# Kernel tuning notes

Hardware: AMD Instinct MI355X
Metric: run time of the kernel (lower is better)

Reference implementation:

```python
import jax, jax.numpy as jnp
import numpy as np

B, T, D, H = 8192, 64, 100, 110  # batch, t_grid_size, W_dim, 10+W_dim
S = T - 1                        # number of subnets / loop steps
SIG, R, DCOEF = 0.3, 0.1, 0.1
NUM_TIME_INTERVAL = 1.0
EPS = 1e-6


def setup_inputs() -> dict:
    key = jax.random.key(0)
    ks = jax.random.split(key, 16)
    f32 = jnp.float32
    inp = {
        "W": jax.random.normal(ks[0], (B, T, D), f32),
        "y_init": jax.random.uniform(ks[1], (1,), f32, 0.0, 1.0),
        "z_init": jax.random.uniform(ks[2], (1,), f32, -0.1, 0.1),
        # BatchNorm params: gamma ~ U(0.1,0.5), beta ~ N(0, 0.1) as in the keras initializers
        "g0": jax.random.uniform(ks[3], (S, D + 1), f32, 0.1, 0.5),
        "b0": 0.1 * jax.random.normal(ks[4], (S, D + 1), f32),
        "g1": jax.random.uniform(ks[5], (S, H), f32, 0.1, 0.5),
        "b1": 0.1 * jax.random.normal(ks[6], (S, H), f32),
        "g2": jax.random.uniform(ks[7], (S, H), f32, 0.1, 0.5),
        "b2": 0.1 * jax.random.normal(ks[8], (S, H), f32),
        "g3": jax.random.uniform(ks[9], (S, D), f32, 0.1, 0.5),
        "b3": 0.1 * jax.random.normal(ks[10], (S, D), f32),
        # Dense weights (glorot-ish scale); first two have no bias, last has bias
        "w0": jax.random.normal(ks[11], (S, D + 1, H), f32) / np.sqrt(D + 1),
        "w1": jax.random.normal(ks[12], (S, H, H), f32) / np.sqrt(H),
        "w2": jax.random.normal(ks[13], (S, H, D), f32) / np.sqrt(H),
        "bias2": jnp.zeros((S, D), f32),
    }
    return inp


def _bn(z, gamma, beta):
    # training-mode batch norm over batch axis (keras axis=1 -> per-feature)
    mu = jnp.mean(z, axis=0, keepdims=True)
    var = jnp.var(z, axis=0, keepdims=True)
    return gamma * (z - mu) * jax.lax.rsqrt(var + EPS) + beta


def reference(W, y_init, z_init, g0, b0, g1, b1, g2, b2, g3, b3, w0, w1, w2, bias2):
    delta_t = NUM_TIME_INTERVAL / T
    dW = jnp.transpose(W[:, 1:, :] - W[:, :-1, :], (1, 0, 2))  # [S, B, D]
    t_idx = jnp.arange(S, dtype=W.dtype)
    exp_coef = jnp.exp(-3.0 * R * (1.0 - t_idx * delta_t))      # [S]

    x0 = jnp.full((B, D), np.pi / 2, W.dtype)
    y0 = jnp.ones((B, 1), W.dtype) * y_init
    z0 = jnp.ones((B, D), W.dtype) * z_init

    def drift(x, y, ec):
        s = jnp.sum(jnp.sin(x), axis=1, keepdims=True)
        return -R * y + 0.5 * SIG ** 2 * ec * (DCOEF * s) ** 3

    def step(carry, xs):
        x, y, z = carry
        dw, ec, pg0, pb0, pg1, pb1, pg2, pb2, pg3, pb3, pw0, pw1, pw2, pbb = xs
        x = x + SIG * dw * y
        y = y - drift(x, y, ec) * delta_t + jnp.sum(z * dw, axis=1, keepdims=True)
        h = jnp.concatenate([x, y], axis=1)          # [B, D+1]
        h = _bn(h, pg0, pb0)
        h = jax.nn.relu(_bn(h @ pw0, pg1, pb1))      # [B, H]
        h = jax.nn.relu(_bn(h @ pw1, pg2, pb2))      # [B, H]
        z = _bn(h @ pw2 + pbb, pg3, pb3) / D         # [B, D]
        return (x, y, z), None

    xs = (dW, exp_coef, g0, b0, g1, b1, g2, b2, g3, b3, w0, w1, w2, bias2)
    (x, y, z), _ = jax.lax.scan(step, (x0, y0, z0), xs)

    # final step: Python loop leaves t = T-2; increment W[:,-1]-W[:,-2] == dW[-1]
    dw_last = dW[-1]
    x = x + SIG * y * dw_last
    y = y - drift(x, y, exp_coef[-1]) * delta_t + jnp.sum(z * dw_last, axis=1, keepdims=True)
    return (x, y)
```

## Files before the change

kernel.cpp:

```cpp
#include <hip/hip_runtime.h>
#include <cstdint>
#include <cstddef>

#define NBLK 128
#define NT   256
#define ROWS 64
#define DD   100
#define HH   110
#define NS   63
#define NGRP 16
#define GRP  (NBLK / NGRP)
#define REGF 512

typedef __bf16 bf16x8 __attribute__((ext_vector_type(8)));
typedef float  f32x16 __attribute__((ext_vector_type(16)));

struct Params {
  const float* W; const float* yini; const float* zini;
  const float* g0; const float* b0; const float* g1; const float* b1;
  const float* g2; const float* b2; const float* g3; const float* b3;
  const float* w0; const float* w1; const float* w2;
  float* out; float* slots; int* cnts;
};

__device__ __forceinline__ float agent_ld(const float* p_) {
  return __hip_atomic_load(p_, __ATOMIC_RELAXED, __HIP_MEMORY_SCOPE_AGENT);
}
__device__ __forceinline__ void agent_st(float* p_, float v) {
  __hip_atomic_store(p_, v, __ATOMIC_RELAXED, __HIP_MEMORY_SCOPE_AGENT);
}

__device__ __forceinline__ void sync_arrive(int* cn) {
  asm volatile("s_waitcnt vmcnt(0)" ::: "memory");
  __syncthreads();
  if (threadIdx.x == 0)
    __hip_atomic_fetch_add(&cn[(blockIdx.x & (NGRP - 1)) * 16], 1,
                           __ATOMIC_RELAXED, __HIP_MEMORY_SCOPE_AGENT);
}
__device__ __forceinline__ void sync_wait(int* cn, int target) {
  if (threadIdx.x < NGRP) {
    while (__hip_atomic_load(&cn[threadIdx.x * 16], __ATOMIC_RELAXED,
                             __HIP_MEMORY_SCOPE_AGENT) < target)
      __builtin_amdgcn_s_sleep(1);
  }
  __syncthreads();
  asm volatile("" ::: "memory");
}

template<int K, int N>
__device__ __forceinline__ void issueB(const float* wg, int n, int half, float (*t)[8]) {
#pragma unroll
  for (int c = 0; c < 7; ++c) {
#pragma unroll
    for (int j = 0; j < 8; ++j) {
      int k = c * 16 + half * 8 + j;
      t[c][j] = (k < K && n < N) ? wg[k * N + n] : 0.f;
    }
  }
}

__device__ __forceinline__ void run_mfma2(const __bf16* hs, const float (*t)[8],
                                          int col, int half, f32x16* acc) {
  acc[0] = (f32x16)(0.f);
  acc[1] = (f32x16)(0.f);
#pragma unroll
  for (int c = 0; c < 7; ++c) {
    bf16x8 bfv;
#pragma unroll
    for (int j = 0; j < 8; ++j) bfv[j] = (__bf16)t[c][j];
    bf16x8 a0 = *(const bf16x8*)(hs + col * 120 + c * 16 + half * 8);
    bf16x8 a1 = *(const bf16x8*)(hs + (32 + col) * 120 + c * 16 + half * 8);
    acc[0] = __builtin_amdgcn_mfma_f32_32x32x16_bf16(a0, bfv, acc[0], 0, 0, 0);
    acc[1] = __builtin_amdgcn_mfma_f32_32x32x16_bf16(a1, bfv, acc[1], 0, 0, 0);
  }
}

__device__ __forceinline__ void frag2(const f32x16* acc, float* slot, int n, int N, int half) {
  float sm = 0.f, sq = 0.f;
#pragma unroll
  for (int m = 0; m < 2; ++m)
#pragma unroll
    for (int i = 0; i < 16; ++i) { float v = acc[m][i]; sm += v; sq += v * v; }
  sm += __shfl_xor(sm, 32);
  sq += __shfl_xor(sq, 32);
  if (half == 0 && n < N) {
    atomicAdd(&slot[n], sm);
    atomicAdd(&slot[112 + n], sq);
  }
}

__device__ __forceinline__ void frag3(const f32x16* acc, float* slot, int n, int half,
                                      const float* ysl) {
  float sm = 0.f, sq = 0.f, sy = 0.f;
#pragma unroll
  for (int m = 0; m < 2; ++m)
#pragma unroll
    for (int i = 0; i < 16; ++i) {
      float v = acc[m][i];
      int row = m * 32 + (i & 3) + 8 * (i >> 2) + 4 * half;
      sm += v; sq += v * v; sy += v * ysl[row];
    }
  sm += __shfl_xor(sm, 32);
  sq += __shfl_xor(sq, 32);
  sy += __shfl_xor(sy, 32);
  if (half == 0 && n < HH) {
    atomicAdd(&slot[n], sm);
    atomicAdd(&slot[112 + n], sq);
    atomicAdd(&slot[224 + n], sy);
  }
}

__device__ __forceinline__ void finalize2(const float* slot, const float* gam,
                                          const float* bet, int n, int N, float scale,
                                          float& a, float& c) {
  a = 0.f; c = 0.f;
  if (n < N) {
    float sm = agent_ld(&slot[n]);
    float sq = agent_ld(&slot[112 + n]);
    float mean = sm * (1.f / 8192.f);
    float var  = fmaxf(sq * (1.f / 8192.f) - mean * mean, 0.f);
    float au = gam[n] * rsqrtf(var + 1e-6f);
    a = au * scale;
    c = (bet[n] - mean * au) * scale;
  }
}

__device__ __forceinline__ void write_h(__bf16* hs, const f32x16* acc,
                                        float a, float c, int n, int half) {
  if (n < 112) {
#pragma unroll
    for (int m = 0; m < 2; ++m)
#pragma unroll
      for (int i = 0; i < 16; ++i) {
        int row = m * 32 + (i & 3) + 8 * (i >> 2) + 4 * half;
        float v = fmaxf(acc[m][i] * a + c, 0.f);
        hs[row * 120 + n] = (__bf16)v;
      }
  }
}

__device__ __forceinline__ void write_h1(__bf16* hs, const f32x16* acc,
                                         float a, float c, float ay, float cy,
                                         float w0yn, int n, int half, const float* ysl) {
  if (n < 112) {
#pragma unroll
    for (int m = 0; m < 2; ++m)
#pragma unroll
      for (int i = 0; i < 16; ++i) {
        int row = m * 32 + (i & 3) + 8 * (i >> 2) + 4 * half;
        float add = (ay * ysl[row] + cy) * w0yn;
        float v = fmaxf((acc[m][i] + add) * a + c, 0.f);
        hs[row * 120 + n] = (__bf16)v;
      }
  }
}

__device__ __forceinline__ void write_z(float* zsl, const f32x16* acc,
                                        float a, float c, int n, int half) {
  if (n < DD) {
#pragma unroll
    for (int m = 0; m < 2; ++m)
#pragma unroll
      for (int i = 0; i < 16; ++i) {
        int row = m * 32 + (i & 3) + 8 * (i >> 2) + 4 * half;
        zsl[row * 104 + n] = acc[m][i] * a + c;
      }
  }
}

__global__ __launch_bounds__(NT) void bsde_kernel(Params p) {
  __shared__ float xs[ROWS * 104];
  __shared__ float zs[ROWS * 104];
  __shared__ float dws[ROWS * 104];
  __shared__ float ys[ROWS];
  __shared__ float us[ROWS];
  __shared__ __bf16 hsb[ROWS * 120];
  __shared__ float aS[128], cS[128];

  const int tid  = threadIdx.x;
  const int lane = tid & 63;
  const int wv   = tid >> 6;
  const int col  = lane & 31;
  const int half = lane >> 5;
  const int n    = wv * 32 + col;
  const int b0   = blockIdx.x * ROWS;

  {
    float z0 = p.zini[0];
    for (int i = tid; i < ROWS * 104; i += NT) { xs[i] = 1.57079632679f; zs[i] = z0; }
    for (int i = tid; i < ROWS * 120; i += NT) hsb[i] = (__bf16)0.f;
    if (tid < ROWS) ys[tid] = p.yini[0];
  }
  for (int idx = tid; idx < ROWS * 128; idx += NT) {
    int r = idx >> 7, d = idx & 127;
    if (d < DD) {
      const float* wr = p.W + (size_t)(b0 + r) * 6400 + d;
      dws[r * 104 + d] = wr[100] - wr[0];
    }
  }
  __syncthreads();

  int seg = 0;
  float tB[7][8];
  float w0yn;

  {
    int r = tid >> 2, l4 = tid & 3;
    float yr = ys[r];
    float ssum = 0.f;
#pragma unroll
    for (int i = 0; i < 25; ++i) {
      int d = l4 + 4 * i;
      float dw = dws[r * 104 + d];
      float xv = xs[r * 104 + d] + 0.3f * dw * yr;
      xs[r * 104 + d] = xv;
      ssum += __sinf(xv);
    }
    ssum += __shfl_down(ssum, 2, 4);
    ssum += __shfl_down(ssum, 1, 4);
    if (l4 == 0) {
      float ec = __expf(-0.3f);
      float tc = 0.1f * ssum;
      float drift = -0.1f * yr + 0.045f * ec * tc * tc * tc;
      us[r] = yr - drift * (1.f / 64.f);
    }
  }
  __syncthreads();
  {
    float* slot = p.slots + (seg % 3) * REGF;
    if (tid < DD) {
      float sm = 0.f, sq = 0.f;
      for (int r = 0; r < ROWS; ++r) { float v = xs[r * 104 + tid]; sm += v; sq += v * v; }
      atomicAdd(&slot[224 + tid], sm);
      atomicAdd(&slot[336 + tid], sq);
    }
    sync_arrive(p.cnts);
    issueB<DD, HH>(p.w0, n, half, tB);
    w0yn = (n < HH) ? p.w0[100 * 110 + n] : 0.f;
    sync_wait(p.cnts, (seg + 1) * GRP);
    if (blockIdx.x < 2)
      agent_st(&p.slots[((seg + 2) % 3) * REGF + (int)blockIdx.x * 256 + tid], 0.f);
    if (tid < DD) {
      float sm = agent_ld(&slot[224 + tid]);
      float sq = agent_ld(&slot[336 + tid]);
      float mean = sm * (1.f / 8192.f);
      float var  = fmaxf(sq * (1.f / 8192.f) - mean * mean, 0.f);
      float au = p.g0[tid] * rsqrtf(var + 1e-6f);
      aS[tid] = au; cS[tid] = p.b0[tid] - mean * au;
    }
    ++seg;
  }
  __syncthreads();

  for (int s = 0; s < NS; ++s) {
    {
      int r = tid >> 2, l4 = tid & 3;
      float zdw = 0.f;
#pragma unroll
      for (int i = 0; i < 25; ++i) {
        int d = l4 + 4 * i;
        zdw += zs[r * 104 + d] * dws[r * 104 + d];
      }
      zdw += __shfl_down(zdw, 2, 4);
      zdw += __shfl_down(zdw, 1, 4);
      if (l4 == 0) ys[r] = us[r] + zdw;
    }
    __syncthreads();
    float* Eslot = p.slots + (seg % 3) * REGF;
    if (tid < 64) {
      float v = ys[tid], v2 = v * v;
#pragma unroll
      for (int off = 32; off > 0; off >>= 1) {
        v  += __shfl_down(v, off);
        v2 += __shfl_down(v2, off);
      }
      if (tid == 0) { atomicAdd(&Eslot[336], v); atomicAdd(&Eslot[337], v2); }
    }
    for (int idx = tid; idx < ROWS * 128; idx += NT) {
      int r = idx >> 7, d = idx & 127;
      if (d < DD) hsb[r * 120 + d] = (__bf16)(xs[r * 104 + d] * aS[d] + cS[d]);
    }
    __syncthreads();

    f32x16 acc[2];
    run_mfma2(hsb, tB, col, half, acc);
    frag3(acc, Eslot, n, half, ys);
    sync_arrive(p.cnts);
    issueB<HH, HH>(p.w1 + (size_t)s * 12100, n, half, tB);
    sync_wait(p.cnts, (seg + 1) * GRP);
    if (blockIdx.x < 2)
      agent_st(&p.slots[((seg + 2) % 3) * REGF + (int)blockIdx.x * 256 + tid], 0.f);
    float ay, cy, a1 = 0.f, c1 = 0.f;
    {
      float Sy  = agent_ld(&Eslot[336]);
      float Syy = agent_ld(&Eslot[337]);
      float my = Sy * (1.f / 8192.f);
      float vy = fmaxf(Syy * (1.f / 8192.f) - my * my, 0.f);
      float auy = p.g0[s * 101 + 100] * rsqrtf(vy + 1e-6f);
      ay = auy; cy = p.b0[s * 101 + 100] - my * auy;
      if (n < HH) {
        float G1 = agent_ld(&Eslot[n]);
        float G2 = agent_ld(&Eslot[112 + n]);
        float G3 = agent_ld(&Eslot[224 + n]);
        float Sv  = ay * Sy + 8192.f * cy;
        float Svv = ay * ay * Syy + 2.f * ay * cy * Sy + 8192.f * cy * cy;
        float w = w0yn;
        float S1 = G1 + w * Sv;
        float S2 = G2 + 2.f * w * (ay * G3 + cy * G1) + w * w * Svv;
        float mean = S1 * (1.f / 8192.f);
        float var  = fmaxf(S2 * (1.f / 8192.f) - mean * mean, 0.f);
        float au = p.g1[s * HH + n] * rsqrtf(var + 1e-6f);
        a1 = au; c1 = p.b1[s * HH + n] - mean * au;
      }
    }
    ++seg;
    write_h1(hsb, acc, a1, c1, ay, cy, w0yn, n, half, ys);
    __syncthreads();

    run_mfma2(hsb, tB, col, half, acc);
    float* Cslot = p.slots + (seg % 3) * REGF;
    frag2(acc, Cslot, n, HH, half);
    sync_arrive(p.cnts);
    issueB<HH, DD>(p.w2 + (size_t)s * 11000, n, half, tB);
    if (s + 1 < NS) {
      for (int idx = tid; idx < ROWS * 128; idx += NT) {
        int r = idx >> 7, d = idx & 127;
        if (d < DD) {
          const float* wr = p.W + (size_t)(b0 + r) * 6400 + (s + 1) * 100 + d;
          dws[r * 104 + d] = wr[100] - wr[0];
        }
      }
      w0yn = (n < HH) ? p.w0[(size_t)(s + 1) * 11110 + 11000 + n] : 0.f;
    }
    sync_wait(p.cnts, (seg + 1) * GRP);
    if (blockIdx.x < 2)
      agent_st(&p.slots[((seg + 2) % 3) * REGF + (int)blockIdx.x * 256 + tid], 0.f);
    float a2, c2;
    finalize2(Cslot, p.g2 + s * HH, p.b2 + s * HH, n, HH, 1.f, a2, c2);
    ++seg;
    write_h(hsb, acc, a2, c2, n, half);
    __syncthreads();
    run_mfma2(hsb, tB, col, half, acc);
    float* Dslot = p.slots + (seg % 3) * REGF;
    frag2(acc, Dslot, n, DD, half);
    {
      int r = tid >> 2, l4 = tid & 3;
      float yr = ys[r];
      float ssum = 0.f;
#pragma unroll
      for (int i = 0; i < 25; ++i) {
        int d = l4 + 4 * i;
        float dw = dws[r * 104 + d];
        float xv = xs[r * 104 + d] + 0.3f * dw * yr;
        xs[r * 104 + d] = xv;
        ssum += __sinf(xv);
      }
      ssum += __shfl_down(ssum, 2, 4);
      ssum += __shfl_down(ssum, 1, 4);
      if (l4 == 0) {
        int ei = (s + 1 < NS) ? s + 1 : NS - 1;
        float ec = __expf(-0.3f * (1.f - (float)ei * (1.f / 64.f)));
        float tc = 0.1f * ssum;
        float drift = -0.1f * yr + 0.045f * ec * tc * tc * tc;
        us[r] = yr - drift * (1.f / 64.f);
      }
    }
    __syncthreads();
    if (tid < DD) {
      float sm = 0.f, sq = 0.f;
      for (int r = 0; r < ROWS; ++r) { float v = xs[r * 104 + tid]; sm += v; sq += v * v; }
      atomicAdd(&Dslot[224 + tid], sm);
      atomicAdd(&Dslot[336 + tid], sq);
    }
    sync_arrive(p.cnts);
    if (s + 1 < NS) issueB<DD, HH>(p.w0 + (size_t)(s + 1) * 11110, n, half, tB);
    sync_wait(p.cnts, (seg + 1) * GRP);
    if (blockIdx.x < 2)
      agent_st(&p.slots[((seg + 2) % 3) * REGF + (int)blockIdx.x * 256 + tid], 0.f);
    float a3, c3;
    finalize2(Dslot, p.g3 + s * DD, p.b3 + s * DD, n, DD, 0.01f, a3, c3);
    if (s + 1 < NS && tid < DD) {
      float sm = agent_ld(&Dslot[224 + tid]);
      float sq = agent_ld(&Dslot[336 + tid]);
      float mean = sm * (1.f / 8192.f);
      float var  = fmaxf(sq * (1.f / 8192.f) - mean * mean, 0.f);
      float au = p.g0[(s + 1) * 101 + tid] * rsqrtf(var + 1e-6f);
      aS[tid] = au; cS[tid] = p.b0[(s + 1) * 101 + tid] - mean * au;
    }
    ++seg;
    write_z(zs, acc, a3, c3, n, half);
    __syncthreads();
  }

  {
    int r = tid >> 2, l4 = tid & 3;
    float zdw = 0.f;
#pragma unroll
    for (int i = 0; i < 25; ++i) {
      int d = l4 + 4 * i;
      zdw += zs[r * 104 + d] * dws[r * 104 + d];
    }
    zdw += __shfl_down(zdw, 2, 4);
    zdw += __shfl_down(zdw, 1, 4);
    if (l4 == 0) ys[r] = us[r] + zdw;
  }
  __syncthreads();

  for (int idx = tid; idx < ROWS * 128; idx += NT) {
    int r = idx >> 7, d = idx & 127;
    if (d < DD) p.out[(size_t)(b0 + r) * 100 + d] = xs[r * 104 + d];
  }
  if (tid < ROWS) p.out[819200 + b0 + tid] = ys[tid];
}

extern "C" void kernel_launch(void* const* d_in, const int* in_sizes, int n_in,
                              void* d_out, int out_size, void* d_ws, size_t ws_size,
                              hipStream_t stream) {
  Params p;
  p.W    = (const float*)d_in[0];
  p.yini = (const float*)d_in[1];
  p.zini = (const float*)d_in[2];
  p.g0   = (const float*)d_in[3];  p.b0 = (const float*)d_in[4];
  p.g1   = (const float*)d_in[5];  p.b1 = (const float*)d_in[6];
  p.g2   = (const float*)d_in[7];  p.b2 = (const float*)d_in[8];
  p.g3   = (const float*)d_in[9];  p.b3 = (const float*)d_in[10];
  p.w0   = (const float*)d_in[11]; p.w1 = (const float*)d_in[12];
  p.w2   = (const float*)d_in[13];
  p.out   = (float*)d_out;
  p.slots = (float*)d_ws;
  p.cnts  = (int*)((char*)d_ws + (size_t)3 * REGF * 4);

  size_t zbytes = (size_t)3 * REGF * 4
                + (size_t)NGRP * 16 * 4;
  hipMemsetAsync(d_ws, 0, zbytes, stream);
  bsde_kernel<<<dim3(NBLK), dim3(NT), 0, stream>>>(p);
}
```

Measured before the change: 3.116 ms.

## Replace flat grid barrier with hierarchical group/super counter and release flags

Changes the grid-wide barrier from each block polling all 16 group counters with 16 threads to a two-level tree. The last arriver in each group bumps a super counter, and the final group writes per-group release flags that each block polls with a single thread. It also loads the y-statistics once per block into shared memory instead of every thread doing agent-scope loads. The aim is less polling traffic and contention on the barrier counters, at the cost of a longer serial chain of atomics on the critical arrival path.

```diff
diff --git a/kernel.cpp b/kernel.cpp
--- a/kernel.cpp
+++ b/kernel.cpp
@@ -20,7 +20,7 @@
   const float* g0; const float* b0; const float* g1; const float* b1;
   const float* g2; const float* b2; const float* g3; const float* b3;
   const float* w0; const float* w1; const float* w2;
-  float* out; float* slots; int* cnts;
+  float* out; float* slots; int* gcnt; int* scnt; int* rel;
 };
 
 __device__ __forceinline__ float agent_ld(const float* p_) {
@@ -30,17 +30,29 @@
   __hip_atomic_store(p_, v, __ATOMIC_RELAXED, __HIP_MEMORY_SCOPE_AGENT);
 }
 
-__device__ __forceinline__ void sync_arrive(int* cn) {
+__device__ __forceinline__ void sync_arrive(int* gcnt, int* scnt, int* rel, int bar) {
   asm volatile("s_waitcnt vmcnt(0)" ::: "memory");
   __syncthreads();
-  if (threadIdx.x == 0)
-    __hip_atomic_fetch_add(&cn[(blockIdx.x & (NGRP - 1)) * 16], 1,
-                           __ATOMIC_RELAXED, __HIP_MEMORY_SCOPE_AGENT);
-}
-__device__ __forceinline__ void sync_wait(int* cn, int target) {
-  if (threadIdx.x < NGRP) {
-    while (__hip_atomic_load(&cn[threadIdx.x * 16], __ATOMIC_RELAXED,
-                             __HIP_MEMORY_SCOPE_AGENT) < target)
+  if (threadIdx.x == 0) {
+    int g = blockIdx.x & (NGRP - 1);
+    int old = __hip_atomic_fetch_add(&gcnt[g * 16], 1,
+                                     __ATOMIC_RELAXED, __HIP_MEMORY_SCOPE_AGENT);
+    if (old == GRP * (bar + 1) - 1) {
+      int so = __hip_atomic_fetch_add(scnt, 1,
+                                      __ATOMIC_RELAXED, __HIP_MEMORY_SCOPE_AGENT);
+      if (so == NGRP * (bar + 1) - 1) {
+#pragma unroll
+        for (int i = 0; i < NGRP; ++i)
+          __hip_atomic_store(&rel[i * 16], bar + 1,
+                             __ATOMIC_RELAXED, __HIP_MEMORY_SCOPE_AGENT);
+      }
+    }
+  }
+}
+__device__ __forceinline__ void sync_wait(const int* rel, int bar) {
+  if (threadIdx.x == 0) {
+    while (__hip_atomic_load(&rel[(blockIdx.x & (NGRP - 1)) * 16],
+                             __ATOMIC_RELAXED, __HIP_MEMORY_SCOPE_AGENT) < bar + 1)
       __builtin_amdgcn_s_sleep(1);
   }
   __syncthreads();
@@ -176,6 +188,7 @@
   __shared__ float us[ROWS];
   __shared__ __bf16 hsb[ROWS * 120];
   __shared__ float aS[128], cS[128];
+  __shared__ float syS[2];
 
   const int tid  = threadIdx.x;
   const int lane = tid & 63;
@@ -234,10 +247,10 @@
       atomicAdd(&slot[224 + tid], sm);
       atomicAdd(&slot[336 + tid], sq);
     }
-    sync_arrive(p.cnts);
+    sync_arrive(p.gcnt, p.scnt, p.rel, seg);
     issueB<DD, HH>(p.w0, n, half, tB);
     w0yn = (n < HH) ? p.w0[100 * 110 + n] : 0.f;
-    sync_wait(p.cnts, (seg + 1) * GRP);
+    sync_wait(p.rel, seg);
     if (blockIdx.x < 2)
       agent_st(&p.slots[((seg + 2) % 3) * REGF + (int)blockIdx.x * 256 + tid], 0.f);
     if (tid < DD) {
@@ -285,15 +298,17 @@
     f32x16 acc[2];
     run_mfma2(hsb, tB, col, half, acc);
     frag3(acc, Eslot, n, half, ys);
-    sync_arrive(p.cnts);
+    sync_arrive(p.gcnt, p.scnt, p.rel, seg);
     issueB<HH, HH>(p.w1 + (size_t)s * 12100, n, half, tB);
-    sync_wait(p.cnts, (seg + 1) * GRP);
+    sync_wait(p.rel, seg);
     if (blockIdx.x < 2)
       agent_st(&p.slots[((seg + 2) % 3) * REGF + (int)blockIdx.x * 256 + tid], 0.f);
+    if (tid == 0) { syS[0] = agent_ld(&Eslot[336]); syS[1] = agent_ld(&Eslot[337]); }
+    __syncthreads();
     float ay, cy, a1 = 0.f, c1 = 0.f;
     {
-      float Sy  = agent_ld(&Eslot[336]);
-      float Syy = agent_ld(&Eslot[337]);
+      float Sy  = syS[0];
+      float Syy = syS[1];
       float my = Sy * (1.f / 8192.f);
       float vy = fmaxf(Syy * (1.f / 8192.f) - my * my, 0.f);
       float auy = p.g0[s * 101 + 100] * rsqrtf(vy + 1e-6f);
@@ -320,7 +335,7 @@
     run_mfma2(hsb, tB, col, half, acc);
     float* Cslot = p.slots + (seg % 3) * REGF;
     frag2(acc, Cslot, n, HH, half);
-    sync_arrive(p.cnts);
+    sync_arrive(p.gcnt, p.scnt, p.rel, seg);
     issueB<HH, DD>(p.w2 + (size_t)s * 11000, n, half, tB);
     if (s + 1 < NS) {
       for (int idx = tid; idx < ROWS * 128; idx += NT) {
@@ -332,7 +347,7 @@
       }
       w0yn = (n < HH) ? p.w0[(size_t)(s + 1) * 11110 + 11000 + n] : 0.f;
     }
-    sync_wait(p.cnts, (seg + 1) * GRP);
+    sync_wait(p.rel, seg);
     if (blockIdx.x < 2)
       agent_st(&p.slots[((seg + 2) % 3) * REGF + (int)blockIdx.x * 256 + tid], 0.f);
     float a2, c2;
@@ -372,9 +387,9 @@
       atomicAdd(&Dslot[224 + tid], sm);
       atomicAdd(&Dslot[336 + tid], sq);
     }
-    sync_arrive(p.cnts);
+    sync_arrive(p.gcnt, p.scnt, p.rel, seg);
     if (s + 1 < NS) issueB<DD, HH>(p.w0 + (size_t)(s + 1) * 11110, n, half, tB);
-    sync_wait(p.cnts, (seg + 1) * GRP);
+    sync_wait(p.rel, seg);
     if (blockIdx.x < 2)
       agent_st(&p.slots[((seg + 2) % 3) * REGF + (int)blockIdx.x * 256 + tid], 0.f);
     float a3, c3;
@@ -428,10 +443,12 @@
   p.w2   = (const float*)d_in[13];
   p.out   = (float*)d_out;
   p.slots = (float*)d_ws;
-  p.cnts  = (int*)((char*)d_ws + (size_t)3 * REGF * 4);
-
-  size_t zbytes = (size_t)3 * REGF * 4
-                + (size_t)NGRP * 16 * 4;
+  char* base = (char*)d_ws + (size_t)3 * REGF * 4;
+  p.gcnt = (int*)base;
+  p.scnt = (int*)(base + 1024);
+  p.rel  = (int*)(base + 1088);
+
+  size_t zbytes = (size_t)3 * REGF * 4 + 1024 + 64 + 1024;
   hipMemsetAsync(d_ws, 0, zbytes, stream);
   bsde_kernel<<<dim3(NBLK), dim3(NT), 0, stream>>>(p);
 }
```

Measured after the change: 3.115 ms. Within noise of the previous version (-0.0%).
